# Kernel tuning notes

Hardware: AMD Instinct MI355X
Metric: run time of the kernel (lower is better)

Reference implementation:

```python
import jax, jax.numpy as jnp
import numpy as np

E, T, IN, OUT = 8, 16384, 1024, 1024  # n_groups, total_tokens, in_features, out_features


def setup_inputs() -> dict:
    key = jax.random.key(0)
    kx, kw, ks = jax.random.split(key, 3)
    x = jax.random.normal(kx, (T, IN), dtype=jnp.float32)
    # kaiming_uniform-ish scale for weight [E, OUT, IN]
    weight = jax.random.normal(kw, (E, OUT, IN), dtype=jnp.float32) * (1.0 / np.sqrt(IN))
    # ragged segment lengths that sum exactly to T (random cut points)
    cuts = jnp.sort(jax.random.randint(ks, (E - 1,), 0, T + 1)).astype(jnp.int32)
    seg_lens = jnp.diff(
        jnp.concatenate([jnp.zeros((1,), jnp.int32), cuts, jnp.full((1,), T, jnp.int32)])
    )
    return {"x": x, "weight": weight, "seg_lens": seg_lens}


def reference(x, weight, seg_lens):
    # Grouped GEMM: row t of x is multiplied by weight[g(t)].T where g(t) is the
    # segment (expert) that token t falls into per seg_lens. trans_b=True.
    n_groups = weight.shape[0]
    bounds = jnp.cumsum(seg_lens)                                  # [E]
    seg_id = jnp.searchsorted(bounds, jnp.arange(x.shape[0]), side="right")  # [T]
    y = jnp.zeros((x.shape[0], weight.shape[1]), dtype=x.dtype)
    for e in range(n_groups):  # small fixed loop over groups
        y = y + jnp.where((seg_id == e)[:, None], x @ weight[e].T, 0)
    return y
```

## Files before the change

### kernel.cpp

```cpp
#include <hip/hip_runtime.h>

#define T_TOK  16384
#define IN_F   1024
#define OUT_F  1024
#define NE     8
#define BM     128
#define BN     128
#define BK     32
#define NTHREADS 256
#define ROW_TILE_SLOTS 136

typedef __bf16 bf16;
typedef bf16  bf16x4 __attribute__((ext_vector_type(4)));
typedef bf16  bf16x8 __attribute__((ext_vector_type(8)));
typedef float f32x4  __attribute__((ext_vector_type(4)));

#define NX_CHUNKS (T_TOK * IN_F / 4)
#define NW_CHUNKS (NE * OUT_F * IN_F / 4)
#define NTOT_CHUNKS (NX_CHUNKS + NW_CHUNKS)

__global__ __launch_bounds__(NTHREADS)
void cvt_f32_to_bf16(const float* __restrict__ x, const float* __restrict__ w,
                     bf16* __restrict__ xb, bf16* __restrict__ wb)
{
    for (int i = blockIdx.x * NTHREADS + threadIdx.x; i < NTOT_CHUNKS;
         i += gridDim.x * NTHREADS) {
        const bool isx = (i < NX_CHUNKS);
        const int  j   = isx ? i : i - NX_CHUNKS;
        f32x4 v = isx ? ((const f32x4*)x)[j] : ((const f32x4*)w)[j];
        bf16x4 h;
        #pragma unroll
        for (int k = 0; k < 4; ++k) h[k] = (bf16)v[k];
        if (isx) ((bf16x4*)xb)[j] = h;
        else     ((bf16x4*)wb)[j] = h;
    }
}

__device__ __forceinline__ void gld_lds16(const bf16* g, bf16* l) {
    __builtin_amdgcn_global_load_lds(
        (const __attribute__((address_space(1))) void*)g,
        (__attribute__((address_space(3))) void*)l,
        16, 0, 0);
}

__global__ __launch_bounds__(NTHREADS)
void grouped_gemm_bf16(const bf16* __restrict__ xb,
                       const bf16* __restrict__ wb,
                       const int*  __restrict__ seg_lens,
                       float* __restrict__ out)
{
    __shared__ __align__(16) bf16 As[BM * BK];
    __shared__ __align__(16) bf16 Bs[BN * BK];

    const int m    = blockIdx.y;
    const int col0 = blockIdx.x * BN;

    int e_sel = -1, row0 = 0, rows = 0;
    {
        int start = 0, acct = 0;
        #pragma unroll
        for (int e = 0; e < NE; ++e) {
            int len = seg_lens[e];
            int nt  = (len + BM - 1) >> 7;
            if (e_sel < 0 && m >= acct && m < acct + nt) {
                e_sel = e;
                row0  = start + (m - acct) * BM;
                int rem = start + len - row0;
                rows = rem < BM ? rem : BM;
            }
            acct  += nt;
            start += len;
        }
    }
    if (e_sel < 0) return;

    const int tid  = threadIdx.x;
    const int lane = tid & 63;
    const int wave = tid >> 6;
    const int wm   = (wave >> 1) * 64;
    const int wn   = (wave & 1) * 64;
    const int quad = lane >> 4;
    const int l16  = lane & 15;

    const bf16* wbase = wb + ((size_t)e_sel * OUT_F + (size_t)col0) * IN_F;

    const int grp0 = wave * 16 + (lane >> 2);
    const int kofs = (lane & 3) * 8;
    int rgA0 = row0 + grp0;          if (rgA0 > T_TOK - 1) rgA0 = T_TOK - 1;
    int rgA1 = row0 + grp0 + 64;     if (rgA1 > T_TOK - 1) rgA1 = T_TOK - 1;
    const bf16* gA0 = xb + (size_t)rgA0 * IN_F + kofs;
    const bf16* gA1 = xb + (size_t)rgA1 * IN_F + kofs;
    const bf16* gB0 = wbase + (size_t)grp0 * IN_F + kofs;
    const bf16* gB1 = wbase + (size_t)(grp0 + 64) * IN_F + kofs;
    bf16* lA0 = As + wave * 512;
    bf16* lA1 = As + (4 + wave) * 512;
    bf16* lB0 = Bs + wave * 512;
    bf16* lB1 = Bs + (4 + wave) * 512;

    f32x4 acc[4][4] = {};

    for (int k0 = 0; k0 < IN_F; k0 += BK) {
        gld_lds16(gA0 + k0, lA0);
        gld_lds16(gA1 + k0, lA1);
        gld_lds16(gB0 + k0, lB0);
        gld_lds16(gB1 + k0, lB1);
        __syncthreads();

        bf16x8 af[4], bfr[4];
        #pragma unroll
        for (int t = 0; t < 4; ++t)
            af[t] = *(const bf16x8*)(&As[(wm + t * 16 + l16) * BK + quad * 8]);
        #pragma unroll
        for (int u = 0; u < 4; ++u)
            bfr[u] = *(const bf16x8*)(&Bs[(wn + u * 16 + l16) * BK + quad * 8]);

        #pragma unroll
        for (int t = 0; t < 4; ++t)
            #pragma unroll
            for (int u = 0; u < 4; ++u)
                acc[t][u] = __builtin_amdgcn_mfma_f32_16x16x32_bf16(
                    af[t], bfr[u], acc[t][u], 0, 0, 0);

        __syncthreads();
    }

    #pragma unroll
    for (int t = 0; t < 4; ++t) {
        #pragma unroll
        for (int r = 0; r < 4; ++r) {
            int row = wm + t * 16 + quad * 4 + r;
            if (row < rows) {
                size_t ob = (size_t)(row0 + row) * OUT_F + col0;
                #pragma unroll
                for (int u = 0; u < 4; ++u)
                    out[ob + wn + u * 16 + l16] = acc[t][u][r];
            }
        }
    }
}

__global__ __launch_bounds__(NTHREADS)
void grouped_gemm_f32io_bf16(const float* __restrict__ x,
                             const float* __restrict__ wgt,
                             const int*  __restrict__ seg_lens,
                             float* __restrict__ out)
{
    __shared__ __align__(16) bf16 As[BM * BK];
    __shared__ __align__(16) bf16 Bs[BN * BK];

    const int m    = blockIdx.y;
    const int col0 = blockIdx.x * BN;

    int e_sel = -1, row0 = 0, rows = 0;
    {
        int start = 0, acct = 0;
        #pragma unroll
        for (int e = 0; e < NE; ++e) {
            int len = seg_lens[e];
            int nt  = (len + BM - 1) >> 7;
            if (e_sel < 0 && m >= acct && m < acct + nt) {
                e_sel = e;
                row0  = start + (m - acct) * BM;
                int rem = start + len - row0;
                rows = rem < BM ? rem : BM;
            }
            acct  += nt;
            start += len;
        }
    }
    if (e_sel < 0) return;

    const int tid  = threadIdx.x;
    const int lane = tid & 63;
    const int wave = tid >> 6;
    const int wm   = (wave >> 1) * 64;
    const int wn   = (wave & 1) * 64;
    const int quad = lane >> 4;
    const int l16  = lane & 15;

    const float* wbase = wgt + ((size_t)e_sel * OUT_F + (size_t)col0) * IN_F;

    f32x4 acc[4][4] = {};

    for (int k0 = 0; k0 < IN_F; k0 += BK) {
        f32x4 a_st[4], b_st[4];
        #pragma unroll
        for (int t = 0; t < 4; ++t) {
            int c  = t * NTHREADS + tid;
            int rg = row0 + (c >> 3);
            if (rg > T_TOK - 1) rg = T_TOK - 1;
            a_st[t] = *(const f32x4*)(x + (size_t)rg * IN_F + k0 + (c & 7) * 4);
            b_st[t] = *(const f32x4*)(wbase + (size_t)(c >> 3) * IN_F + k0 + (c & 7) * 4);
        }

        __syncthreads();

        #pragma unroll
        for (int t = 0; t < 4; ++t) {
            int c = t * NTHREADS + tid;
            bf16x4 ha, hb;
            #pragma unroll
            for (int j = 0; j < 4; ++j) { ha[j] = (bf16)a_st[t][j]; hb[j] = (bf16)b_st[t][j]; }
            *(bf16x4*)(&As[(c >> 3) * BK + (c & 7) * 4]) = ha;
            *(bf16x4*)(&Bs[(c >> 3) * BK + (c & 7) * 4]) = hb;
        }
        __syncthreads();

        bf16x8 af[4], bfr[4];
        #pragma unroll
        for (int t = 0; t < 4; ++t)
            af[t] = *(const bf16x8*)(&As[(wm + t * 16 + l16) * BK + quad * 8]);
        #pragma unroll
        for (int u = 0; u < 4; ++u)
            bfr[u] = *(const bf16x8*)(&Bs[(wn + u * 16 + l16) * BK + quad * 8]);

        #pragma unroll
        for (int t = 0; t < 4; ++t)
            #pragma unroll
            for (int u = 0; u < 4; ++u)
                acc[t][u] = __builtin_amdgcn_mfma_f32_16x16x32_bf16(
                    af[t], bfr[u], acc[t][u], 0, 0, 0);
    }

    #pragma unroll
    for (int t = 0; t < 4; ++t) {
        #pragma unroll
        for (int r = 0; r < 4; ++r) {
            int row = wm + t * 16 + quad * 4 + r;
            if (row < rows) {
                size_t ob = (size_t)(row0 + row) * OUT_F + col0;
                #pragma unroll
                for (int u = 0; u < 4; ++u)
                    out[ob + wn + u * 16 + l16] = acc[t][u][r];
            }
        }
    }
}

extern "C" void kernel_launch(void* const* d_in, const int* in_sizes, int n_in,
                              void* d_out, int out_size, void* d_ws, size_t ws_size,
                              hipStream_t stream) {
    const float* x   = (const float*)d_in[0];
    const float* wgt = (const float*)d_in[1];
    const int*   seg = (const int*)d_in[2];
    float* out = (float*)d_out;

    const size_t xbytes = (size_t)T_TOK * IN_F * sizeof(bf16);
    const size_t wbytes = (size_t)NE * OUT_F * IN_F * sizeof(bf16);

    dim3 grid(OUT_F / BN, ROW_TILE_SLOTS, 1);
    dim3 block(NTHREADS, 1, 1);

    if (ws_size >= xbytes + wbytes) {
        bf16* xb = (bf16*)d_ws;
        bf16* wb = (bf16*)((char*)d_ws + xbytes);
        cvt_f32_to_bf16<<<dim3(2048, 1, 1), block, 0, stream>>>(x, wgt, xb, wb);
        grouped_gemm_bf16<<<grid, block, 0, stream>>>(xb, wb, seg, out);
    } else {
        grouped_gemm_f32io_bf16<<<grid, block, 0, stream>>>(x, wgt, seg, out);
    }
}
```

Baseline: 218.7 us.

## Use 256x256x64 tiles with double-buffered LDS prefetch in grouped GEMM

Replaces the 128x128x32 bf16 grouped GEMM with a 512-thread kernel using 256x256 output tiles, BK=64, and double-buffered LDS where the next k-slice is loaded via global_load_lds while the current one is computed. The aim is more reuse per loaded byte, fewer barriers per FLOP, and overlap of loads with MFMA work. In exchange each wave holds 32 accumulators (high register pressure), LDS use is 128KB, and the grid shrinks to 4x72 blocks. Ragged segment edges also waste more rows with 256-row tiles. The f32 fallback kernel is left functionally unchanged and only renamed.

```diff
diff --git a/kernel.cpp b/kernel.cpp
--- a/kernel.cpp
+++ b/kernel.cpp
@@ -4,27 +4,23 @@
 #define IN_F   1024
 #define OUT_F  1024
 #define NE     8
-#define BM     128
-#define BN     128
-#define BK     32
-#define NTHREADS 256
-#define ROW_TILE_SLOTS 136
 
 typedef __bf16 bf16;
 typedef bf16  bf16x4 __attribute__((ext_vector_type(4)));
 typedef bf16  bf16x8 __attribute__((ext_vector_type(8)));
 typedef float f32x4  __attribute__((ext_vector_type(4)));
 
+#define CVT_THREADS 256
 #define NX_CHUNKS (T_TOK * IN_F / 4)
 #define NW_CHUNKS (NE * OUT_F * IN_F / 4)
 #define NTOT_CHUNKS (NX_CHUNKS + NW_CHUNKS)
 
-__global__ __launch_bounds__(NTHREADS)
+__global__ __launch_bounds__(CVT_THREADS)
 void cvt_f32_to_bf16(const float* __restrict__ x, const float* __restrict__ w,
                      bf16* __restrict__ xb, bf16* __restrict__ wb)
 {
-    for (int i = blockIdx.x * NTHREADS + threadIdx.x; i < NTOT_CHUNKS;
-         i += gridDim.x * NTHREADS) {
+    for (int i = blockIdx.x * CVT_THREADS + threadIdx.x; i < NTOT_CHUNKS;
+         i += gridDim.x * CVT_THREADS) {
         const bool isx = (i < NX_CHUNKS);
         const int  j   = isx ? i : i - NX_CHUNKS;
         f32x4 v = isx ? ((const f32x4*)x)[j] : ((const f32x4*)w)[j];
@@ -35,6 +31,12 @@
         else     ((bf16x4*)wb)[j] = h;
     }
 }
+
+#define BM 256
+#define BN 256
+#define BK 64
+#define GTHREADS 512
+#define ROW_SLOTS 72
 
 __device__ __forceinline__ void gld_lds16(const bf16* g, bf16* l) {
     __builtin_amdgcn_global_load_lds(
@@ -43,14 +45,14 @@
         16, 0, 0);
 }
 
-__global__ __launch_bounds__(NTHREADS)
-void grouped_gemm_bf16(const bf16* __restrict__ xb,
-                       const bf16* __restrict__ wb,
-                       const int*  __restrict__ seg_lens,
-                       float* __restrict__ out)
+__global__ __launch_bounds__(GTHREADS)
+void grouped_gemm_bf16_256(const bf16* __restrict__ xb,
+                           const bf16* __restrict__ wb,
+                           const int*  __restrict__ seg_lens,
+                           float* __restrict__ out)
 {
-    __shared__ __align__(16) bf16 As[BM * BK];
-    __shared__ __align__(16) bf16 Bs[BN * BK];
+    __shared__ __align__(16) bf16 As[2][BM * BK];
+    __shared__ __align__(16) bf16 Bs[2][BN * BK];
 
     const int m    = blockIdx.y;
     const int col0 = blockIdx.x * BN;
@@ -61,12 +63,130 @@
         #pragma unroll
         for (int e = 0; e < NE; ++e) {
             int len = seg_lens[e];
-            int nt  = (len + BM - 1) >> 7;
+            int nt  = (len + BM - 1) >> 8;
             if (e_sel < 0 && m >= acct && m < acct + nt) {
                 e_sel = e;
                 row0  = start + (m - acct) * BM;
                 int rem = start + len - row0;
                 rows = rem < BM ? rem : BM;
+            }
+            acct  += nt;
+            start += len;
+        }
+    }
+    if (e_sel < 0) return;
+
+    const int tid  = threadIdx.x;
+    const int lane = tid & 63;
+    const int wave = tid >> 6;
+    const int wr   = wave >> 2;
+    const int wc   = wave & 3;
+    const int quad = lane >> 4;
+    const int l16  = lane & 15;
+
+    const bf16* wbase = wb + ((size_t)e_sel * OUT_F + (size_t)col0) * IN_F;
+
+    const int rq = lane >> 3;
+    const int ke = (lane & 7) * 8;
+    const bf16* ga[4];
+    const bf16* gb[4];
+    #pragma unroll
+    for (int i = 0; i < 4; ++i) {
+        int q  = wave * 4 + i;
+        int ra = row0 + q * 8 + rq;
+        if (ra > T_TOK - 1) ra = T_TOK - 1;
+        ga[i] = xb + (size_t)ra * IN_F + ke;
+        gb[i] = wbase + (size_t)(q * 8 + rq) * IN_F + ke;
+    }
+    const int q0 = wave * 4;
+
+    f32x4 acc[8][4] = {};
+
+    #pragma unroll
+    for (int i = 0; i < 4; ++i) {
+        gld_lds16(ga[i], &As[0][(q0 + i) * 512]);
+        gld_lds16(gb[i], &Bs[0][(q0 + i) * 512]);
+    }
+    __syncthreads();
+
+    int cur = 0;
+    for (int ks = 0; ks < IN_F / BK; ++ks) {
+        const int kn = (ks + 1) * BK;
+        if (kn < IN_F) {
+            #pragma unroll
+            for (int i = 0; i < 4; ++i) {
+                gld_lds16(ga[i] + kn, &As[cur ^ 1][(q0 + i) * 512]);
+                gld_lds16(gb[i] + kn, &Bs[cur ^ 1][(q0 + i) * 512]);
+            }
+        }
+
+        #pragma unroll
+        for (int kk = 0; kk < 2; ++kk) {
+            bf16x8 af[8], bfr[4];
+            #pragma unroll
+            for (int t = 0; t < 8; ++t)
+                af[t] = *(const bf16x8*)(
+                    &As[cur][(wr * 128 + t * 16 + l16) * BK + kk * 32 + quad * 8]);
+            #pragma unroll
+            for (int u = 0; u < 4; ++u)
+                bfr[u] = *(const bf16x8*)(
+                    &Bs[cur][(wc * 64 + u * 16 + l16) * BK + kk * 32 + quad * 8]);
+            #pragma unroll
+            for (int t = 0; t < 8; ++t)
+                #pragma unroll
+                for (int u = 0; u < 4; ++u)
+                    acc[t][u] = __builtin_amdgcn_mfma_f32_16x16x32_bf16(
+                        af[t], bfr[u], acc[t][u], 0, 0, 0);
+        }
+
+        __syncthreads();
+        cur ^= 1;
+    }
+
+    #pragma unroll
+    for (int t = 0; t < 8; ++t) {
+        #pragma unroll
+        for (int r = 0; r < 4; ++r) {
+            int row = wr * 128 + t * 16 + quad * 4 + r;
+            if (row < rows) {
+                size_t ob = (size_t)(row0 + row) * OUT_F + col0 + wc * 64;
+                #pragma unroll
+                for (int u = 0; u < 4; ++u)
+                    out[ob + u * 16 + l16] = acc[t][u][r];
+            }
+        }
+    }
+}
+
+#define FBM 128
+#define FBK 32
+#define FTHREADS 256
+#define FROW_SLOTS 136
+
+__global__ __launch_bounds__(FTHREADS)
+void grouped_gemm_f32io_bf16(const float* __restrict__ x,
+                             const float* __restrict__ wgt,
+                             const int*  __restrict__ seg_lens,
+                             float* __restrict__ out)
+{
+    __shared__ __align__(16) bf16 Asf[FBM * FBK];
+    __shared__ __align__(16) bf16 Bsf[FBM * FBK];
+
+    const int m    = blockIdx.y;
+    const int col0 = blockIdx.x * FBM;
+
+    int e_sel = -1, row0 = 0, rows = 0;
+    {
+        int start = 0, acct = 0;
+        #pragma unroll
+        for (int e = 0; e < NE; ++e) {
+            int len = seg_lens[e];
+            int nt  = (len + FBM - 1) >> 7;
+            if (e_sel < 0 && m >= acct && m < acct + nt) {
+                e_sel = e;
+                row0  = start + (m - acct) * FBM;
+                int rem = start + len - row0;
+                rows = rem < FBM ? rem : FBM;
             }
             acct  += nt;
             start += len;
@@ -82,37 +202,41 @@
     const int quad = lane >> 4;
     const int l16  = lane & 15;
 
-    const bf16* wbase = wb + ((size_t)e_sel * OUT_F + (size_t)col0) * IN_F;
-
-    const int grp0 = wave * 16 + (lane >> 2);
-    const int kofs = (lane & 3) * 8;
-    int rgA0 = row0 + grp0;          if (rgA0 > T_TOK - 1) rgA0 = T_TOK - 1;
-    int rgA1 = row0 + grp0 + 64;     if (rgA1 > T_TOK - 1) rgA1 = T_TOK - 1;
-    const bf16* gA0 = xb + (size_t)rgA0 * IN_F + kofs;
-    const bf16* gA1 = xb + (size_t)rgA1 * IN_F + kofs;
-    const bf16* gB0 = wbase + (size_t)grp0 * IN_F + kofs;
-    const bf16* gB1 = wbase + (size_t)(grp0 + 64) * IN_F + kofs;
-    bf16* lA0 = As + wave * 512;
-    bf16* lA1 = As + (4 + wave) * 512;
-    bf16* lB0 = Bs + wave * 512;
-    bf16* lB1 = Bs + (4 + wave) * 512;
+    const float* wbase = wgt + ((size_t)e_sel * OUT_F + (size_t)col0) * IN_F;
 
     f32x4 acc[4][4] = {};
 
-    for (int k0 = 0; k0 < IN_F; k0 += BK) {
-        gld_lds16(gA0 + k0, lA0);
-        gld_lds16(gA1 + k0, lA1);
-        gld_lds16(gB0 + k0, lB0);
-        gld_lds16(gB1 + k0, lB1);
+    for (int k0 = 0; k0 < IN_F; k0 += FBK) {
+        f32x4 a_st[4], b_st[4];
+        #pragma unroll
+        for (int t = 0; t < 4; ++t) {
+            int c  = t * FTHREADS + tid;
+            int rg = row0 + (c >> 3);
+            if (rg > T_TOK - 1) rg = T_TOK - 1;
+            a_st[t] = *(const f32x4*)(x + (size_t)rg * IN_F + k0 + (c & 7) * 4);
+            b_st[t] = *(const f32x4*)(wbase + (size_t)(c >> 3) * IN_F + k0 + (c & 7) * 4);
+        }
+
         __syncthreads();
 
+        #pragma unroll
+        for (int t = 0; t < 4; ++t) {
+            int c = t * FTHREADS + tid;
+            bf16x4 ha, hb;
+            #pragma unroll
+            for (int j = 0; j < 4; ++j) { ha[j] = (bf16)a_st[t][j]; hb[j] = (bf16)b_st[t][j]; }
+            *(bf16x4*)(&Asf[(c >> 3) * FBK + (c & 7) * 4]) = ha;
+            *(bf16x4*)(&Bsf[(c >> 3) * FBK + (c & 7) * 4]) = hb;
+        }
+        __syncthreads();
+
         bf16x8 af[4], bfr[4];
         #pragma unroll
         for (int t = 0; t < 4; ++t)
-            af[t] = *(const bf16x8*)(&As[(wm + t * 16 + l16) * BK + quad * 8]);
+            af[t] = *(const bf16x8*)(&Asf[(wm + t * 16 + l16) * FBK + quad * 8]);
         #pragma unroll
         for (int u = 0; u < 4; ++u)
-            bfr[u] = *(const bf16x8*)(&Bs[(wn + u * 16 + l16) * BK + quad * 8]);
+            bfr[u] = *(const bf16x8*)(&Bsf[(wn + u * 16 + l16) * FBK + quad * 8]);
 
         #pragma unroll
         for (int t = 0; t < 4; ++t)
@@ -120,8 +244,6 @@
             for (int u = 0; u < 4; ++u)
                 acc[t][u] = __builtin_amdgcn_mfma_f32_16x16x32_bf16(
                     af[t], bfr[u], acc[t][u], 0, 0, 0);
-
-        __syncthreads();
     }
 
     #pragma unroll
@@ -139,104 +261,6 @@
     }
 }
 
-__global__ __launch_bounds__(NTHREADS)
-void grouped_gemm_f32io_bf16(const float* __restrict__ x,
-                             const float* __restrict__ wgt,
-                             const int*  __restrict__ seg_lens,
-                             float* __restrict__ out)
-{
-    __shared__ __align__(16) bf16 As[BM * BK];
-    __shared__ __align__(16) bf16 Bs[BN * BK];
-
-    const int m    = blockIdx.y;
-    const int col0 = blockIdx.x * BN;
-
-    int e_sel = -1, row0 = 0, rows = 0;
-    {
-        int start = 0, acct = 0;
-        #pragma unroll
-        for (int e = 0; e < NE; ++e) {
-            int len = seg_lens[e];
-            int nt  = (len + BM - 1) >> 7;
-            if (e_sel < 0 && m >= acct && m < acct + nt) {
-                e_sel = e;
-                row0  = start + (m - acct) * BM;
-                int rem = start + len - row0;
-                rows = rem < BM ? rem : BM;
-            }
-            acct  += nt;
-            start += len;
-        }
-    }
-    if (e_sel < 0) return;
-
-    const int tid  = threadIdx.x;
-    const int lane = tid & 63;
-    const int wave = tid >> 6;
-    const int wm   = (wave >> 1) * 64;
-    const int wn   = (wave & 1) * 64;
-    const int quad = lane >> 4;
-    const int l16  = lane & 15;
-
-    const float* wbase = wgt + ((size_t)e_sel * OUT_F + (size_t)col0) * IN_F;
-
-    f32x4 acc[4][4] = {};
-
-    for (int k0 = 0; k0 < IN_F; k0 += BK) {
-        f32x4 a_st[4], b_st[4];
-        #pragma unroll
-        for (int t = 0; t < 4; ++t) {
-            int c  = t * NTHREADS + tid;
-            int rg = row0 + (c >> 3);
-            if (rg > T_TOK - 1) rg = T_TOK - 1;
-            a_st[t] = *(const f32x4*)(x + (size_t)rg * IN_F + k0 + (c & 7) * 4);
-            b_st[t] = *(const f32x4*)(wbase + (size_t)(c >> 3) * IN_F + k0 + (c & 7) * 4);
-        }
-
-        __syncthreads();
-
-        #pragma unroll
-        for (int t = 0; t < 4; ++t) {
-            int c = t * NTHREADS + tid;
-            bf16x4 ha, hb;
-            #pragma unroll
-            for (int j = 0; j < 4; ++j) { ha[j] = (bf16)a_st[t][j]; hb[j] = (bf16)b_st[t][j]; }
-            *(bf16x4*)(&As[(c >> 3) * BK + (c & 7) * 4]) = ha;
-            *(bf16x4*)(&Bs[(c >> 3) * BK + (c & 7) * 4]) = hb;
-        }
-        __syncthreads();
-
-        bf16x8 af[4], bfr[4];
-        #pragma unroll
-        for (int t = 0; t < 4; ++t)
-            af[t] = *(const bf16x8*)(&As[(wm + t * 16 + l16) * BK + quad * 8]);
-        #pragma unroll
-        for (int u = 0; u < 4; ++u)
-            bfr[u] = *(const bf16x8*)(&Bs[(wn + u * 16 + l16) * BK + quad * 8]);
-
-        #pragma unroll
-        for (int t = 0; t < 4; ++t)
-            #pragma unroll
-            for (int u = 0; u < 4; ++u)
-                acc[t][u] = __builtin_amdgcn_mfma_f32_16x16x32_bf16(
-                    af[t], bfr[u], acc[t][u], 0, 0, 0);
-    }
-
-    #pragma unroll
-    for (int t = 0; t < 4; ++t) {
-        #pragma unroll
-        for (int r = 0; r < 4; ++r) {
-            int row = wm + t * 16 + quad * 4 + r;
-            if (row < rows) {
-                size_t ob = (size_t)(row0 + row) * OUT_F + col0;
-                #pragma unroll
-                for (int u = 0; u < 4; ++u)
-                    out[ob + wn + u * 16 + l16] = acc[t][u][r];
-            }
-        }
-    }
-}
-
 extern "C" void kernel_launch(void* const* d_in, const int* in_sizes, int n_in,
                               void* d_out, int out_size, void* d_ws, size_t ws_size,
                               hipStream_t stream) {
@@ -248,15 +272,15 @@
     const size_t xbytes = (size_t)T_TOK * IN_F * sizeof(bf16);
     const size_t wbytes = (size_t)NE * OUT_F * IN_F * sizeof(bf16);
 
-    dim3 grid(OUT_F / BN, ROW_TILE_SLOTS, 1);
-    dim3 block(NTHREADS, 1, 1);
-
     if (ws_size >= xbytes + wbytes) {
         bf16* xb = (bf16*)d_ws;
         bf16* wb = (bf16*)((char*)d_ws + xbytes);
-        cvt_f32_to_bf16<<<dim3(2048, 1, 1), block, 0, stream>>>(x, wgt, xb, wb);
-        grouped_gemm_bf16<<<grid, block, 0, stream>>>(xb, wb, seg, out);
+        cvt_f32_to_bf16<<<dim3(2048, 1, 1), dim3(CVT_THREADS, 1, 1), 0, stream>>>(
+            x, wgt, xb, wb);
+        grouped_gemm_bf16_256<<<dim3(OUT_F / BN, ROW_SLOTS, 1),
+                                dim3(GTHREADS, 1, 1), 0, stream>>>(xb, wb, seg, out);
     } else {
-        grouped_gemm_f32io_bf16<<<grid, block, 0, stream>>>(x, wgt, seg, out);
-    }
-}
+        grouped_gemm_f32io_bf16<<<dim3(OUT_F / FBM, FROW_SLOTS, 1),
+                                  dim3(FTHREADS, 1, 1), 0, stream>>>(x, wgt, seg, out);
+    }
+}
```

New measurement: 232.1 us. +6.1%, slower.
